# Kernel optimization log

Measured on AMD Instinct MI355X. Metric: run time of the kernel, lower is better.

## Reference

```python
import jax, jax.numpy as jnp
import numpy as np

S = 3
K = 3
K2 = K * K
BN_EPS = 1e-5


def _conv(x, w, pad=0):
    return jax.lax.conv_general_dilated(
        x, w, window_strides=(1, 1), padding=[(pad, pad), (pad, pad)],
        dimension_numbers=('NCHW', 'OIHW', 'NCHW'))


def _adaptive_avg_pool(x, s):
    # PyTorch adaptive_avg_pool2d semantics: bin i covers [floor(i*H/s), ceil((i+1)*H/s))
    B, C, H, W = x.shape
    rows = []
    for i in range(s):
        h0, h1 = (i * H) // s, -(-((i + 1) * H) // s)
        cols = []
        for j in range(s):
            w0, w1 = (j * W) // s, -(-((j + 1) * W) // s)
            cols.append(x[:, :, h0:h1, w0:w1].mean(axis=(2, 3)))
        rows.append(jnp.stack(cols, axis=-1))
    return jnp.stack(rows, axis=-2)  # (B, C, s, s)


def _forward(c4, c5, w_to_fuse, bn_gamma, bn_beta, w_c4_proc, w_conv1,
             w_reshape, w_proj, w_sim4, w_sim5, kg_w1, kg_b1, kg_w2, kg_b2,
             mask_raw):
    B, C4, H, W = c4.shape
    H2, W2 = c5.shape[2], c5.shape[3]
    # nearest upsample c5 -> (H, W)
    ih = (jnp.arange(H) * H2) // H
    iw = (jnp.arange(W) * W2) // W
    c5_up = c5[:, :, ih][:, :, :, iw]

    c4_proc = _conv(c4, w_c4_proc, pad=1)
    c5_proc = _conv(c5_up, w_conv1)  # adaptive pool to (H,W) is identity here
    fused = c4_proc + c5_proc

    # to_fuse 1x1 conv -> BatchNorm (training-mode batch stats) -> SiLU
    y = _conv(fused, w_to_fuse)
    mu = y.mean(axis=(0, 2, 3), keepdims=True)
    var = y.var(axis=(0, 2, 3), keepdims=True)
    y = (y - mu) / jnp.sqrt(var + BN_EPS)
    X = jax.nn.silu(y * bn_gamma[None, :, None, None] + bn_beta[None, :, None, None])

    # patch descriptors and similarity (dot)
    p4 = _conv(_adaptive_avg_pool(c4, S), w_sim4)    # (B, sim, S, S)
    p5 = _conv(_adaptive_avg_pool(c5_up, S), w_sim5)
    sim = (p4 * p5).sum(axis=1)                      # (B, S, S)

    gated = sim.reshape(B, S * S) * jax.nn.sigmoid(mask_raw)[None, :]  # (B, S2)
    k_in = gated.reshape(B * S * S, 1)
    h = jax.nn.relu(k_in @ kg_w1.T + kg_b1)
    kernels = jax.nn.softmax((h @ kg_w2.T + kg_b2).reshape(B, S * S, K2), axis=-1)

    # unfold X: (B, C, K2, H, W) with torch row-major kernel-position order
    pad = K // 2
    Xp = jnp.pad(X, ((0, 0), (0, 0), (pad, pad), (pad, pad)))
    patches = jnp.stack([Xp[:, :, dy:dy + H, dx:dx + W]
                         for dy in range(K) for dx in range(K)], axis=2)

    # per-pixel patch index -> per-pixel kernel
    y_idx = jnp.clip((jnp.arange(H) * S) // H, 0, S - 1)
    x_idx = jnp.clip((jnp.arange(W) * S) // W, 0, S - 1)
    pidx = y_idx[:, None] * S + x_idx[None, :]       # (H, W) int
    kmap = kernels[:, pidx, :]                       # (B, H, W, K2)

    out = jnp.einsum('bckhw,bhwk->bchw', patches, kmap)

    fused_red = _conv(_conv(fused, w_reshape), w_proj)
    return out + fused_red


def setup_inputs() -> dict:
    key = jax.random.key(0)
    ks = jax.random.split(key, 16)
    B, C4, C5, H, W = 8, 256, 512, 64, 64
    OC, SIM, FR, HID = 256, 64, 128, 16
    n = jax.random.normal
    return {
        'c4': n(ks[0], (B, C4, H, W), dtype=jnp.float32),
        'c5': n(ks[1], (B, C5, H // 2, W // 2), dtype=jnp.float32),
        'w_to_fuse': n(ks[2], (OC, C4, 1, 1), dtype=jnp.float32) * 0.05,
        'bn_gamma': jnp.ones((OC,), dtype=jnp.float32),
        'bn_beta': jnp.zeros((OC,), dtype=jnp.float32),
        'w_c4_proc': n(ks[3], (C4, C4, 3, 3), dtype=jnp.float32) * 0.05,
        'w_conv1': n(ks[4], (C4, C5, 1, 1), dtype=jnp.float32) * 0.05,
        'w_reshape': n(ks[5], (FR, C4, 1, 1), dtype=jnp.float32) * 0.05,
        'w_proj': n(ks[6], (OC, FR, 1, 1), dtype=jnp.float32) * 0.05,
        'w_sim4': n(ks[7], (SIM, C4, 1, 1), dtype=jnp.float32) * 0.05,
        'w_sim5': n(ks[8], (SIM, C5, 1, 1), dtype=jnp.float32) * 0.05,
        'kg_w1': n(ks[9], (HID, 1), dtype=jnp.float32) * 0.5,
        'kg_b1': n(ks[10], (HID,), dtype=jnp.float32) * 0.1,
        'kg_w2': n(ks[11], (K2, HID), dtype=jnp.float32) * 0.5,
        'kg_b2': n(ks[12], (K2,), dtype=jnp.float32) * 0.1,
        'mask_raw': jnp.zeros((K2,), dtype=jnp.float32),
    }


def reference(c4, c5, w_to_fuse, bn_gamma, bn_beta, w_c4_proc, w_conv1,
              w_reshape, w_proj, w_sim4, w_sim5, kg_w1, kg_b1, kg_w2, kg_b2,
              mask_raw):
    return _forward(c4, c5, w_to_fuse, bn_gamma, bn_beta, w_c4_proc, w_conv1,
                    w_reshape, w_proj, w_sim4, w_sim5, kg_w1, kg_b1, kg_w2,
                    kg_b2, mask_raw)
```

## Files before the change

kernel.cpp:

```cpp
#include <hip/hip_runtime.h>
#include <cstddef>

#define B_   8
#define C4_  256
#define C5_  512
#define OC_  256
#define FR_  128
#define H_   64
#define W_   64
#define HW_  4096

typedef unsigned short u16;
typedef __bf16 bf16x8 __attribute__((ext_vector_type(8)));
typedef float floatx16 __attribute__((ext_vector_type(16)));

__device__ __forceinline__ u16 f2b(float x) {
    unsigned int u = __float_as_uint(x);
    return (u16)((u + 0x7FFFu + ((u >> 16) & 1u)) >> 16);
}
__device__ __forceinline__ float b2f(u16 x) {
    return __uint_as_float(((unsigned int)x) << 16);
}

__device__ __forceinline__ void gll16(const u16* g, char* l) {
    __builtin_amdgcn_global_load_lds(
        (const __attribute__((address_space(1))) void*)g,
        (__attribute__((address_space(3))) void*)l, 16, 0, 0);
}

__global__ __launch_bounds__(256) void pack_all(
    const float* __restrict__ w3, const float* __restrict__ w1,
    const float* __restrict__ wtf,
    const float* __restrict__ wp, const float* __restrict__ wr,
    const float* __restrict__ in4, const float* __restrict__ in5,
    u16* __restrict__ A3f, u16* __restrict__ A1f, u16* __restrict__ Wtff,
    u16* __restrict__ Wefff, u16* __restrict__ c4t, u16* __restrict__ c5f,
    float* __restrict__ pool4, float* __restrict__ pool5)
{
    __shared__ float sT[16448];
    const int t = threadIdx.x;
    const int blk = blockIdx.x;

    if (blk < 3072) {
        int i = blk * 256 + t;
        if (i < 589824) {
            int j  = i & 7;
            int l  = (i >> 3) & 63;
            int ks = (i >> 9) & 15;
            int ot = (i >> 13) & 7;
            int tap = i >> 16;
            int oc = ot * 32 + (l & 31);
            int c  = ks * 16 + ((l >> 5) << 3) + j;
            A3f[i] = f2b(w3[((size_t)oc * 256 + c) * 9 + tap]);
        } else if (i < 720896) {
            int i2 = i - 589824;
            int j  = i2 & 7;
            int l  = (i2 >> 3) & 63;
            int ks = (i2 >> 9) & 31;
            int ot = i2 >> 14;
            int oc = ot * 32 + (l & 31);
            int c  = ks * 16 + ((l >> 5) << 3) + j;
            A1f[i2] = f2b(w1[(size_t)oc * 512 + c]);
        } else {
            int i3 = i - 720896;
            int j  = i3 & 7;
            int l  = (i3 >> 3) & 63;
            int ks = (i3 >> 9) & 15;
            int ot = i3 >> 13;
            int oc = ot * 32 + (l & 31);
            int c  = ks * 16 + ((l >> 5) << 3) + j;
            Wtff[i3] = f2b(wtf[(size_t)oc * 256 + c]);
        }
    } else if (blk < 3328) {
        const int oc = blk - 3072, c = t;
        float s = 0.f;
        for (int f = 0; f < 128; ++f)
            s += wp[oc * 128 + f] * wr[f * 256 + c];
        int ot = oc >> 5;
        int lf = (oc & 31) + (((c >> 3) & 1) << 5);
        int ks = c >> 4;
        int j  = c & 7;
        Wefff[(((size_t)ot * 16 + ks) * 64 + lf) * 8 + j] = f2b(s);
    } else {
        const int id = blk - 3328;
        const int b = id / 96, x = id % 96;
        if (x < 64) {
            const int h = x;
            const int w = t & 63, cg = t >> 6;
            for (int i = 0; i < 64; ++i) {
                int c = cg * 64 + i;
                sT[w * 257 + c] = in4[(((size_t)b * 256 + c) * 64 + h) * 64 + w];
            }
            __syncthreads();
            for (int i = 0; i < 16; ++i) {
                int ww = cg * 16 + i;
                int c0 = (t & 63) * 4;
                ushort4 v;
                v.x = f2b(sT[ww * 257 + c0]);
                v.y = f2b(sT[ww * 257 + c0 + 1]);
                v.z = f2b(sT[ww * 257 + c0 + 2]);
                v.w = f2b(sT[ww * 257 + c0 + 3]);
                *(ushort4*)&c4t[(((size_t)b * 66 + h + 1) * 72 + ww + 1) * 256 + c0] = v;
            }
            {
                const int c = t;
                float cs[3];
                #pragma unroll
                for (int j = 0; j < 3; ++j) {
                    const int w0 = (j * 64) / 3, w1 = ((j + 1) * 64 + 2) / 3;
                    float s = 0.f;
                    for (int w2 = w0; w2 < w1; ++w2) s += sT[w2 * 257 + c];
                    cs[j] = s;
                }
                #pragma unroll
                for (int i = 0; i < 3; ++i) {
                    const int h0 = (i * 64) / 3, h1 = ((i + 1) * 64 + 2) / 3;
                    if (h >= h0 && h < h1) {
                        #pragma unroll
                        for (int j = 0; j < 3; ++j)
                            atomicAdd(&pool4[((size_t)b * 256 + c) * 9 + i * 3 + j], cs[j]);
                    }
                }
            }
        } else {
            const int h2 = x - 64;
            const int w = t & 31, cg = t >> 5;
            for (int i = 0; i < 64; ++i) {
                int c = cg * 64 + i;
                sT[w * 513 + c] = in5[(((size_t)b * 512 + c) * 32 + h2) * 32 + w];
            }
            __syncthreads();
            u16* dstb = c5f + (size_t)(b * 32 + h2) * 32768;
            for (int i = 0; i < 32; ++i) {
                int id2 = i * 256 + t;
                int j0 = (id2 & 1) * 4;
                int l  = (id2 >> 1) & 63;
                int ks = (id2 >> 7) & 31;
                int n  = (id2 >> 12) & 1;
                int ch = ks * 16 + ((l >> 5) << 3) + j0;
                int w2 = (n * 32 + (l & 31)) >> 1;
                ushort4 v;
                v.x = f2b(sT[w2 * 513 + ch]);
                v.y = f2b(sT[w2 * 513 + ch + 1]);
                v.z = f2b(sT[w2 * 513 + ch + 2]);
                v.w = f2b(sT[w2 * 513 + ch + 3]);
                *(ushort4*)&dstb[id2 * 4] = v;
            }
            #pragma unroll
            for (int half = 0; half < 2; ++half) {
                const int cc = half * 256 + t;
                float cs[3];
                #pragma unroll
                for (int j = 0; j < 3; ++j) {
                    const int w0 = (j * 64) / 3, w1 = ((j + 1) * 64 + 2) / 3;
                    float s = 0.f;
                    for (int w2 = w0; w2 < w1; ++w2) s += sT[(w2 >> 1) * 513 + cc];
                    cs[j] = s;
                }
                #pragma unroll
                for (int i = 0; i < 3; ++i) {
                    const int h0 = (i * 64) / 3, h1 = ((i + 1) * 64 + 2) / 3;
                    const int wt = (int)(2 * h2 >= h0 && 2 * h2 < h1)
                                 + (int)(2 * h2 + 1 >= h0 && 2 * h2 + 1 < h1);
                    if (wt) {
                        const float fw = (float)wt;
                        #pragma unroll
                        for (int j = 0; j < 3; ++j)
                            atomicAdd(&pool5[((size_t)b * 512 + cc) * 9 + i * 3 + j], fw * cs[j]);
                    }
                }
            }
        }
    }
}

__global__ __launch_bounds__(512, 1) void fuse_all(
    const u16* __restrict__ c4t, const u16* __restrict__ c5f,
    const u16* __restrict__ A3f, const u16* __restrict__ A1f,
    const u16* __restrict__ Wtff, const u16* __restrict__ Wefff,
    u16* __restrict__ yb, u16* __restrict__ outb, float* __restrict__ sums)
{
    extern __shared__ char smem[];
    float* lsum = (float*)(smem + 73728);
    float* lsq  = lsum + 256;

    const int t   = threadIdx.x;
    const int lin = blockIdx.x;
    const int d   = ((lin & 7) << 5) + (lin >> 3);
    const int b   = d >> 5;
    const int rp  = d & 31;
    const int h0  = rp * 2;

    const int l   = t & 63;
    const int w8  = t >> 6;
    const int og  = w8 >> 1;
    const int pg  = w8 & 1;
    const int lc  = l & 31;
    const int lg  = l >> 5;

    const int ocb = og * 64;
    const int otb = og * 2;
    const int gseg = (l & 7) ^ (l >> 3);

    if (t < 256) { lsum[t] = 0.f; lsq[t] = 0.f; }

    floatx16 acc[2][2];
    #pragma unroll
    for (int m = 0; m < 2; ++m)
        #pragma unroll
        for (int n = 0; n < 2; ++n)
            #pragma unroll
            for (int r = 0; r < 16; ++r)
                acc[m][n][r] = 0.f;

    bf16x8 areg[9][2];
    #pragma unroll
    for (int tap = 0; tap < 9; ++tap)
        #pragma unroll
        for (int m = 0; m < 2; ++m)
            areg[tap][m] = *(const bf16x8*)(A3f + ((((size_t)tap * 8 + otb + m) * 16 + 0) * 64 + l) * 8);

    for (int q = w8; q < 36; q += 8) {
        const int r  = q / 9;
        const int cq = (q - r * 9) * 8;
        const u16* gp = c4t + ((((size_t)b * 66 + h0 + r) * 72 + cq + (l >> 3)) << 8)
                      + gseg * 8;
        gll16(gp, smem + (r * 72 + cq) * 128);
    }
    __syncthreads();

    for (int c0 = 0; c0 < 256; c0 += 64) {
        char* bufc = smem + ((c0 >> 6) & 1) * 36864;
        if (c0 < 192) {
            char* bufn = smem + (((c0 >> 6) + 1) & 1) * 36864;
            for (int q = w8; q < 36; q += 8) {
                const int r  = q / 9;
                const int cq = (q - r * 9) * 8;
                const u16* gp = c4t + ((((size_t)b * 66 + h0 + r) * 72 + cq + (l >> 3)) << 8)
                              + c0 + 64 + gseg * 8;
                gll16(gp, bufn + (r * 72 + cq) * 128);
            }
        }

        const int ksb = c0 >> 4;
        #pragma unroll
        for (int kst = 0; kst < 4; ++kst) {
            const int ksgN = (kst < 3) ? (ksb + kst + 1)
                                       : ((c0 < 192) ? ksb + 4 : 0);
            #pragma unroll
            for (int ky = 0; ky < 3; ++ky) {
                #pragma unroll
                for (int kx = 0; kx < 3; ++kx) {
                    const int tap = ky * 3 + kx;
                    bf16x8 bb[2];
                    #pragma unroll
                    for (int n = 0; n < 2; ++n) {
                        const int pix = (pg + ky) * 72 + n * 32 + lc + kx;
                        const int seg = (kst * 2 + lg) ^ (pix & 7);
                        bb[n] = *(const bf16x8*)(bufc + pix * 128 + (seg << 4));
                    }
                    #pragma unroll
                    for (int m = 0; m < 2; ++m)
                        #pragma unroll
                        for (int n = 0; n < 2; ++n)
                            acc[m][n] = __builtin_amdgcn_mfma_f32_32x32x16_bf16(
                                areg[tap][m], bb[n], acc[m][n], 0, 0, 0);
                    #pragma unroll
                    for (int m = 0; m < 2; ++m)
                        areg[tap][m] = *(const bf16x8*)(A3f + ((((size_t)tap * 8 + otb + m) * 16 + ksgN) * 64 + l) * 8);
                }
            }
        }
        __syncthreads();
    }

    const u16* c5b = c5f + (size_t)(b * 32 + rp) * 32768;
    {
        bf16x8 a1[2][2], b1[2][2];
        #pragma unroll
        for (int m = 0; m < 2; ++m) {
            a1[0][m] = *(const bf16x8*)(A1f + ((((size_t)otb + m) * 32 + 0) * 64 + l) * 8);
            b1[0][m] = *(const bf16x8*)(c5b + (((size_t)m * 32 + 0) * 64 + l) * 8);
        }
        #pragma unroll
        for (int ks = 0; ks < 32; ++ks) {
            const int cur = ks & 1, nxt = cur ^ 1;
            if (ks < 31) {
                #pragma unroll
                for (int m = 0; m < 2; ++m) {
                    a1[nxt][m] = *(const bf16x8*)(A1f + ((((size_t)otb + m) * 32 + ks + 1) * 64 + l) * 8);
                    b1[nxt][m] = *(const bf16x8*)(c5b + (((size_t)m * 32 + ks + 1) * 64 + l) * 8);
                }
            }
            #pragma unroll
            for (int m = 0; m < 2; ++m)
                #pragma unroll
                for (int n = 0; n < 2; ++n)
                    acc[m][n] = __builtin_amdgcn_mfma_f32_32x32x16_bf16(
                        a1[cur][m], b1[cur][n], acc[m][n], 0, 0, 0);
        }
    }

    __syncthreads();
    #pragma unroll
    for (int n = 0; n < 2; ++n) {
        const int px = pg * 64 + n * 32 + lc;
        #pragma unroll
        for (int m = 0; m < 2; ++m) {
            #pragma unroll
            for (int rq = 0; rq < 4; ++rq) {
                const int oc = ocb + m * 32 + rq * 8 + lg * 4;
                const int slot = oc >> 3;
                ushort4 v;
                v.x = f2b(acc[m][n][rq * 4 + 0]);
                v.y = f2b(acc[m][n][rq * 4 + 1]);
                v.z = f2b(acc[m][n][rq * 4 + 2]);
                v.w = f2b(acc[m][n][rq * 4 + 3]);
                *(ushort4*)(smem + px * 512 + ((slot ^ (px & 31)) << 4) + (oc & 7) * 2) = v;
            }
        }
    }
    __syncthreads();

    const bool isY = (w8 < 4);
    const u16* Wf  = isY ? Wtff : Wefff;
    u16* dst       = isY ? yb : outb;
    const int ot2  = (w8 & 3) * 2;

    #pragma unroll
    for (int ph = 0; ph < 2; ++ph) {
        floatx16 a2[2][2];
        #pragma unroll
        for (int m = 0; m < 2; ++m)
            #pragma unroll
            for (int n = 0; n < 2; ++n)
                #pragma unroll
                for (int r = 0; r < 16; ++r)
                    a2[m][n][r] = 0.f;

        bf16x8 wreg[2][2];
        #pragma unroll
        for (int m = 0; m < 2; ++m)
            wreg[0][m] = *(const bf16x8*)(Wf + ((((size_t)ot2 + m) * 16 + 0) * 64 + l) * 8);

        #pragma unroll
        for (int ks = 0; ks < 16; ++ks) {
            const int cur = ks & 1, nxt = cur ^ 1;
            if (ks < 15) {
                #pragma unroll
                for (int m = 0; m < 2; ++m)
                    wreg[nxt][m] = *(const bf16x8*)(Wf + ((((size_t)ot2 + m) * 16 + ks + 1) * 64 + l) * 8);
            }
            bf16x8 bb[2];
            #pragma unroll
            for (int n = 0; n < 2; ++n) {
                const int px = ph * 64 + n * 32 + lc;
                const int slot = ks * 2 + lg;
                bb[n] = *(const bf16x8*)(smem + px * 512 + ((slot ^ (px & 31)) << 4));
            }
            #pragma unroll
            for (int m = 0; m < 2; ++m)
                #pragma unroll
                for (int n = 0; n < 2; ++n)
                    a2[m][n] = __builtin_amdgcn_mfma_f32_32x32x16_bf16(
                        wreg[cur][m], bb[n], a2[m][n], 0, 0, 0);
        }

        #pragma unroll
        for (int n = 0; n < 2; ++n) {
            const int px = ph * 64 + n * 32 + lc;
            const int row = px >> 6, wcol = px & 63;
            const size_t gp = (((size_t)b * 64 + h0 + row) * 64 + wcol) * 256;
            #pragma unroll
            for (int m = 0; m < 2; ++m) {
                #pragma unroll
                for (int rq = 0; rq < 4; ++rq) {
                    const int ocl = (w8 & 3) * 64 + m * 32 + rq * 8 + lg * 4;
                    ushort4 v;
                    v.x = f2b(a2[m][n][rq * 4 + 0]);
                    v.y = f2b(a2[m][n][rq * 4 + 1]);
                    v.z = f2b(a2[m][n][rq * 4 + 2]);
                    v.w = f2b(a2[m][n][rq * 4 + 3]);
                    *(ushort4*)&dst[gp + ocl] = v;
                }
            }
        }

        if (isY) {
            #pragma unroll
            for (int m = 0; m < 2; ++m) {
                #pragma unroll
                for (int r = 0; r < 16; ++r) {
                    float s = 0.f, q = 0.f;
                    #pragma unroll
                    for (int n = 0; n < 2; ++n) {
                        float v = a2[m][n][r];
                        s += v; q += v * v;
                    }
                    #pragma unroll
                    for (int off = 1; off < 32; off <<= 1) {
                        s += __shfl_xor(s, off);
                        q += __shfl_xor(q, off);
                    }
                    if (lc == 0) {
                        const int ocl = (w8 & 3) * 64 + m * 32 + (r & 3) + 8 * (r >> 2) + 4 * lg;
                        atomicAdd(&lsum[ocl], s);
                        atomicAdd(&lsq[ocl], q);
                    }
                }
            }
        }
    }

    __syncthreads();
    if (t < 256) {
        atomicAdd(&sums[t], lsum[t]);
        atomicAdd(&sums[256 + t], lsq[t]);
    }
}

__global__ __launch_bounds__(64) void sim_mlp(
    const float* __restrict__ pool4, const float* __restrict__ pool5,
    const float* __restrict__ w4, const float* __restrict__ w5,
    const float* __restrict__ kgw1, const float* __restrict__ kgb1,
    const float* __restrict__ kgw2, const float* __restrict__ kgb2,
    const float* __restrict__ mask, float* __restrict__ kers)
{
    const int r = blockIdx.x, b = blockIdx.y, m = threadIdx.x;
    float p4 = 0.f, p5 = 0.f;
    for (int c = 0; c < C4_; ++c)
        p4 += w4[(size_t)m * C4_ + c] * pool4[((size_t)b * C4_ + c) * 9 + r];
    for (int c = 0; c < C5_; ++c)
        p5 += w5[(size_t)m * C5_ + c] * pool5[((size_t)b * C5_ + c) * 9 + r];
    float v = p4 * p5;
    #pragma unroll
    for (int off = 32; off; off >>= 1) v += __shfl_down(v, off);
    if (m == 0) {
        const int ri = r / 3, rj = r % 3;
        const int h0 = (ri * 64) / 3, h1 = ((ri + 1) * 64 + 2) / 3;
        const int w0 = (rj * 64) / 3, w1 = ((rj + 1) * 64 + 2) / 3;
        const float inv = 1.f / (float)((h1 - h0) * (w1 - w0));
        v *= inv * inv;
        float g = v * (1.f / (1.f + __expf(-mask[r])));
        float hb[16];
        #pragma unroll
        for (int j = 0; j < 16; ++j) hb[j] = fmaxf(g * kgw1[j] + kgb1[j], 0.f);
        float lg[9], mx = -1e30f;
        #pragma unroll
        for (int k = 0; k < 9; ++k) {
            float s = kgb2[k];
            #pragma unroll
            for (int j = 0; j < 16; ++j) s += kgw2[k * 16 + j] * hb[j];
            lg[k] = s;
            mx = fmaxf(mx, s);
        }
        float den = 0.f;
        #pragma unroll
        for (int k = 0; k < 9; ++k) { lg[k] = __expf(lg[k] - mx); den += lg[k]; }
        float inv2 = 1.f / den;
        #pragma unroll
        for (int k = 0; k < 9; ++k)
            kers[((size_t)b * 9 + r) * 9 + k] = lg[k] * inv2;
    }
}

__global__ __launch_bounds__(256) void dynconv_bn(const u16* __restrict__ yb,
                                                  const u16* __restrict__ outb,
                                                  const float* __restrict__ sums,
                                                  const float* __restrict__ gamma,
                                                  const float* __restrict__ beta,
                                                  const float* __restrict__ kers,
                                                  float* __restrict__ out)
{
    __shared__ float sX[4][10][66];
    __shared__ float sK[81];
    __shared__ float sAB[8];
    const int t = threadIdx.x;
    const int lin = blockIdx.x;
    const int dd  = ((lin & 7) << 9) | (lin >> 3);
    const int b   = dd >> 9;
    const int r0  = ((dd >> 6) & 7) * 8;
    const int cg  = dd & 63;
    const int ch = t >> 6, w = t & 63;
    const int c = cg * 4 + ch;

    if (t < 4) {
        const int cc = cg * 4 + t;
        const float n = (float)(B_ * HW_);
        float mu  = sums[cc] / n;
        float var = sums[256 + cc] / n - mu * mu;
        float a = gamma[cc] * rsqrtf(var + 1e-5f);
        sAB[t]     = a;
        sAB[4 + t] = beta[cc] - mu * a;
    }
    if (t < 81) sK[t] = kers[(size_t)b * 81 + t];
    __syncthreads();

    for (int idx = t; idx < 660; idx += 256) {
        int rr = idx / 66, cl = idx % 66;
        int gh = r0 - 1 + rr, gw = cl - 1;
        float v0 = 0.f, v1 = 0.f, v2 = 0.f, v3 = 0.f;
        if (gh >= 0 && gh < H_ && gw >= 0 && gw < W_) {
            ushort4 u = *(const ushort4*)&yb[((((size_t)b * 64 + gh) * 64 + gw) << 8) + cg * 4];
            float z;
            z = fmaf(sAB[0], b2f(u.x), sAB[4]); v0 = z / (1.f + __expf(-z));
            z = fmaf(sAB[1], b2f(u.y), sAB[5]); v1 = z / (1.f + __expf(-z));
            z = fmaf(sAB[2], b2f(u.z), sAB[6]); v2 = z / (1.f + __expf(-z));
            z = fmaf(sAB[3], b2f(u.w), sAB[7]); v3 = z / (1.f + __expf(-z));
        }
        sX[0][rr][cl] = v0;
        sX[1][rr][cl] = v1;
        sX[2][rr][cl] = v2;
        sX[3][rr][cl] = v3;
    }
    __syncthreads();

    const int rx = (w * 3) >> 6;
    for (int hh = 0; hh < 8; ++hh) {
        int h = r0 + hh;
        int ry = (h * 3) >> 6;
        const float* kp = &sK[(ry * 3 + rx) * 9];
        float acc = 0.f;
        #pragma unroll
        for (int dy = 0; dy < 3; ++dy)
            #pragma unroll
            for (int dx = 0; dx < 3; ++dx)
                acc += kp[dy * 3 + dx] * sX[ch][hh + dy][w + dx];
        acc += b2f(outb[((((size_t)b * 64 + h) * 64 + w) << 8) + c]);
        out[(((size_t)b * 256 + c) * H_ + h) * W_ + w] = acc;
    }
}

extern "C" void kernel_launch(void* const* d_in, const int* in_sizes, int n_in,
                              void* d_out, int out_size, void* d_ws, size_t ws_size,
                              hipStream_t stream)
{
    const float* c4       = (const float*)d_in[0];
    const float* c5       = (const float*)d_in[1];
    const float* w_to_fuse= (const float*)d_in[2];
    const float* bn_gamma = (const float*)d_in[3];
    const float* bn_beta  = (const float*)d_in[4];
    const float* w_c4_proc= (const float*)d_in[5];
    const float* w_conv1  = (const float*)d_in[6];
    const float* w_reshape= (const float*)d_in[7];
    const float* w_proj   = (const float*)d_in[8];
    const float* w_sim4   = (const float*)d_in[9];
    const float* w_sim5   = (const float*)d_in[10];
    const float* kg_w1    = (const float*)d_in[11];
    const float* kg_b1    = (const float*)d_in[12];
    const float* kg_w2    = (const float*)d_in[13];
    const float* kg_b2    = (const float*)d_in[14];
    const float* mask_raw = (const float*)d_in[15];

    float* out = (float*)d_out;

    u16*   yb    = (u16*)d_ws;
    u16*   outb  = yb + 8388608;
    u16*   c4t   = outb + 8388608;
    u16*   c5f   = c4t + 9732096;
    u16*   A3f   = c5f + 8388608;
    u16*   A1f   = A3f + 589824;
    u16*   Wtff  = A1f + 131072;
    u16*   Wefff = Wtff + 65536;
    float* pool4 = (float*)(Wefff + 65536);
    float* pool5 = pool4 + 18432;
    float* sums  = pool5 + 36864;
    float* kers  = sums + 512;

    hipMemsetAsync(pool4, 0, (size_t)(18432 + 36864 + 512) * sizeof(float), stream);
    hipMemsetAsync(c4t, 0, (size_t)9732096 * sizeof(u16), stream);

    pack_all<<<4096, 256, 0, stream>>>(w_c4_proc, w_conv1, w_to_fuse,
                                       w_proj, w_reshape, c4, c5,
                                       A3f, A1f, Wtff, Wefff, c4t, c5f,
                                       pool4, pool5);

    fuse_all<<<256, 512, 75776, stream>>>(c4t, c5f, A3f, A1f, Wtff, Wefff,
                                          yb, outb, sums);

    sim_mlp<<<dim3(9, 8), 64, 0, stream>>>(pool4, pool5, w_sim4, w_sim5,
                                           kg_w1, kg_b1, kg_w2, kg_b2,
                                           mask_raw, kers);

    dynconv_bn<<<4096, 256, 0, stream>>>(yb, outb, sums,
                                         bn_gamma, bn_beta, kers, out);
}
```

Measured before the change: 219.9 us.

## Split fused conv kernel to one output row per block, doubling grid

Each fuse_all block now handles a single image row (64 pixels) instead of two, so the grid goes from 256 to 512 blocks. The per-warp tile shrinks from 2x2 to 2x1 MFMA tiles in the 3x3 and c5 stages, the halo buffer shrinks to 3 rows, and the epilogue phase loop collapses to one pass. Launch bounds allow more blocks per CU to raise occupancy and spread work over all CUs. In exchange the 3x3 halo rows (3 per output row instead of 4 per two) and the weight fragments are reloaded more often relative to the compute, lowering reuse.

```diff
diff --git a/kernel.cpp b/kernel.cpp
--- a/kernel.cpp
+++ b/kernel.cpp
@@ -174,44 +174,40 @@
     }
 }
 
-__global__ __launch_bounds__(512, 1) void fuse_all(
+__global__ __launch_bounds__(512, 4) void fuse_all(
     const u16* __restrict__ c4t, const u16* __restrict__ c5f,
     const u16* __restrict__ A3f, const u16* __restrict__ A1f,
     const u16* __restrict__ Wtff, const u16* __restrict__ Wefff,
     u16* __restrict__ yb, u16* __restrict__ outb, float* __restrict__ sums)
 {
     extern __shared__ char smem[];
-    float* lsum = (float*)(smem + 73728);
+    float* lsum = (float*)(smem + 55296);
     float* lsq  = lsum + 256;
 
     const int t   = threadIdx.x;
     const int lin = blockIdx.x;
-    const int d   = ((lin & 7) << 5) + (lin >> 3);
-    const int b   = d >> 5;
-    const int rp  = d & 31;
-    const int h0  = rp * 2;
+    const int d   = ((lin & 7) << 6) + (lin >> 3);
+    const int b   = d >> 6;
+    const int h   = d & 63;
 
     const int l   = t & 63;
     const int w8  = t >> 6;
-    const int og  = w8 >> 1;
-    const int pg  = w8 & 1;
+    const int og  = w8 & 3;
+    const int pxh = w8 >> 2;
     const int lc  = l & 31;
     const int lg  = l >> 5;
 
-    const int ocb = og * 64;
     const int otb = og * 2;
     const int gseg = (l & 7) ^ (l >> 3);
 
     if (t < 256) { lsum[t] = 0.f; lsq[t] = 0.f; }
 
-    floatx16 acc[2][2];
+    floatx16 acc[2];
     #pragma unroll
     for (int m = 0; m < 2; ++m)
         #pragma unroll
-        for (int n = 0; n < 2; ++n)
-            #pragma unroll
-            for (int r = 0; r < 16; ++r)
-                acc[m][n][r] = 0.f;
+        for (int r = 0; r < 16; ++r)
+            acc[m][r] = 0.f;
 
     bf16x8 areg[9][2];
     #pragma unroll
@@ -220,23 +216,23 @@
         for (int m = 0; m < 2; ++m)
             areg[tap][m] = *(const bf16x8*)(A3f + ((((size_t)tap * 8 + otb + m) * 16 + 0) * 64 + l) * 8);
 
-    for (int q = w8; q < 36; q += 8) {
+    for (int q = w8; q < 27; q += 8) {
         const int r  = q / 9;
         const int cq = (q - r * 9) * 8;
-        const u16* gp = c4t + ((((size_t)b * 66 + h0 + r) * 72 + cq + (l >> 3)) << 8)
+        const u16* gp = c4t + ((((size_t)b * 66 + h + r) * 72 + cq + (l >> 3)) << 8)
                       + gseg * 8;
         gll16(gp, smem + (r * 72 + cq) * 128);
     }
     __syncthreads();
 
     for (int c0 = 0; c0 < 256; c0 += 64) {
-        char* bufc = smem + ((c0 >> 6) & 1) * 36864;
+        char* bufc = smem + ((c0 >> 6) & 1) * 27648;
         if (c0 < 192) {
-            char* bufn = smem + (((c0 >> 6) + 1) & 1) * 36864;
-            for (int q = w8; q < 36; q += 8) {
+            char* bufn = smem + (((c0 >> 6) + 1) & 1) * 27648;
+            for (int q = w8; q < 27; q += 8) {
                 const int r  = q / 9;
                 const int cq = (q - r * 9) * 8;
-                const u16* gp = c4t + ((((size_t)b * 66 + h0 + r) * 72 + cq + (l >> 3)) << 8)
+                const u16* gp = c4t + ((((size_t)b * 66 + h + r) * 72 + cq + (l >> 3)) << 8)
                               + c0 + 64 + gseg * 8;
                 gll16(gp, bufn + (r * 72 + cq) * 128);
             }
@@ -252,19 +248,13 @@
                 #pragma unroll
                 for (int kx = 0; kx < 3; ++kx) {
                     const int tap = ky * 3 + kx;
-                    bf16x8 bb[2];
-                    #pragma unroll
-                    for (int n = 0; n < 2; ++n) {
-                        const int pix = (pg + ky) * 72 + n * 32 + lc + kx;
-                        const int seg = (kst * 2 + lg) ^ (pix & 7);
-                        bb[n] = *(const bf16x8*)(bufc + pix * 128 + (seg << 4));
-                    }
+                    const int pix = ky * 72 + pxh * 32 + lc + kx;
+                    const int seg = (kst * 2 + lg) ^ (pix & 7);
+                    bf16x8 bb = *(const bf16x8*)(bufc + pix * 128 + (seg << 4));
                     #pragma unroll
                     for (int m = 0; m < 2; ++m)
-                        #pragma unroll
-                        for (int n = 0; n < 2; ++n)
-                            acc[m][n] = __builtin_amdgcn_mfma_f32_32x32x16_bf16(
-                                areg[tap][m], bb[n], acc[m][n], 0, 0, 0);
+                        acc[m] = __builtin_amdgcn_mfma_f32_32x32x16_bf16(
+                            areg[tap][m], bb, acc[m], 0, 0, 0);
                     #pragma unroll
                     for (int m = 0; m < 2; ++m)
                         areg[tap][m] = *(const bf16x8*)(A3f + ((((size_t)tap * 8 + otb + m) * 16 + ksgN) * 64 + l) * 8);
@@ -274,48 +264,43 @@
         __syncthreads();
     }
 
-    const u16* c5b = c5f + (size_t)(b * 32 + rp) * 32768;
+    const u16* c5b = c5f + (size_t)(b * 32 + (h >> 1)) * 32768;
     {
-        bf16x8 a1[2][2], b1[2][2];
-        #pragma unroll
-        for (int m = 0; m < 2; ++m) {
+        bf16x8 a1[2][2], b1[2];
+        #pragma unroll
+        for (int m = 0; m < 2; ++m)
             a1[0][m] = *(const bf16x8*)(A1f + ((((size_t)otb + m) * 32 + 0) * 64 + l) * 8);
-            b1[0][m] = *(const bf16x8*)(c5b + (((size_t)m * 32 + 0) * 64 + l) * 8);
-        }
+        b1[0] = *(const bf16x8*)(c5b + (((size_t)pxh * 32 + 0) * 64 + l) * 8);
         #pragma unroll
         for (int ks = 0; ks < 32; ++ks) {
             const int cur = ks & 1, nxt = cur ^ 1;
             if (ks < 31) {
                 #pragma unroll
-                for (int m = 0; m < 2; ++m) {
+                for (int m = 0; m < 2; ++m)
                     a1[nxt][m] = *(const bf16x8*)(A1f + ((((size_t)otb + m) * 32 + ks + 1) * 64 + l) * 8);
-                    b1[nxt][m] = *(const bf16x8*)(c5b + (((size_t)m * 32 + ks + 1) * 64 + l) * 8);
-                }
+                b1[nxt] = *(const bf16x8*)(c5b + (((size_t)pxh * 32 + ks + 1) * 64 + l) * 8);
             }
             #pragma unroll
             for (int m = 0; m < 2; ++m)
-                #pragma unroll
-                for (int n = 0; n < 2; ++n)
-                    acc[m][n] = __builtin_amdgcn_mfma_f32_32x32x16_bf16(
-                        a1[cur][m], b1[cur][n], acc[m][n], 0, 0, 0);
+                acc[m] = __builtin_amdgcn_mfma_f32_32x32x16_bf16(
+                    a1[cur][m], b1[cur], acc[m], 0, 0, 0);
         }
     }
 
     __syncthreads();
-    #pragma unroll
-    for (int n = 0; n < 2; ++n) {
-        const int px = pg * 64 + n * 32 + lc;
+    {
+        const int px = pxh * 32 + lc;
         #pragma unroll
         for (int m = 0; m < 2; ++m) {
             #pragma unroll
             for (int rq = 0; rq < 4; ++rq) {
-                const int oc = ocb + m * 32 + rq * 8 + lg * 4;
+                const int oc = og * 64 + m * 32 + rq * 8 + lg * 4;
                 const int slot = oc >> 3;
                 ushort4 v;
-                v.x = f2b(acc[m][n][rq * 4 + 0]);
-                v.y = f2b(acc[m][n][rq * 4 + 1]);
-                v.z = f2b(acc[m][n][rq * 4 + 2]);
-                v.w = f2b(acc[m][n][rq * 4 + 3]);
+                v.x = f2b(acc[m][rq * 4 + 0]);
+                v.y = f2b(acc[m][rq * 4 + 1]);
+                v.z = f2b(acc[m][rq * 4 + 2]);
+                v.w = f2b(acc[m][rq * 4 + 3]);
                 *(ushort4*)(smem + px * 512 + ((slot ^ (px & 31)) << 4) + (oc & 7) * 2) = v;
             }
         }
@@ -327,17 +312,16 @@
     u16* dst       = isY ? yb : outb;
     const int ot2  = (w8 & 3) * 2;
 
+    floatx16 a2[2][2];
     #pragma unroll
-    for (int ph = 0; ph < 2; ++ph) {
-        floatx16 a2[2][2];
-        #pragma unroll
-        for (int m = 0; m < 2; ++m)
-            #pragma unroll
-            for (int n = 0; n < 2; ++n)
-                #pragma unroll
-                for (int r = 0; r < 16; ++r)
-                    a2[m][n][r] = 0.f;
-
+    for (int m = 0; m < 2; ++m)
+        #pragma unroll
+        for (int n = 0; n < 2; ++n)
+            #pragma unroll
+            for (int r = 0; r < 16; ++r)
+                a2[m][n][r] = 0.f;
+
+    {
         bf16x8 wreg[2][2];
         #pragma unroll
         for (int m = 0; m < 2; ++m)
@@ -354,7 +338,7 @@
             bf16x8 bb[2];
             #pragma unroll
             for (int n = 0; n < 2; ++n) {
-                const int px = ph * 64 + n * 32 + lc;
+                const int px = n * 32 + lc;
                 const int slot = ks * 2 + lg;
                 bb[n] = *(const bf16x8*)(smem + px * 512 + ((slot ^ (px & 31)) << 4));
             }
@@ -365,48 +349,47 @@
                     a2[m][n] = __builtin_amdgcn_mfma_f32_32x32x16_bf16(
                         wreg[cur][m], bb[n], a2[m][n], 0, 0, 0);
         }
-
-        #pragma unroll
-        for (int n = 0; n < 2; ++n) {
-            const int px = ph * 64 + n * 32 + lc;
-            const int row = px >> 6, wcol = px & 63;
-            const size_t gp = (((size_t)b * 64 + h0 + row) * 64 + wcol) * 256;
-            #pragma unroll
-            for (int m = 0; m < 2; ++m) {
-                #pragma unroll
-                for (int rq = 0; rq < 4; ++rq) {
-                    const int ocl = (w8 & 3) * 64 + m * 32 + rq * 8 + lg * 4;
-                    ushort4 v;
-                    v.x = f2b(a2[m][n][rq * 4 + 0]);
-                    v.y = f2b(a2[m][n][rq * 4 + 1]);
-                    v.z = f2b(a2[m][n][rq * 4 + 2]);
-                    v.w = f2b(a2[m][n][rq * 4 + 3]);
-                    *(ushort4*)&dst[gp + ocl] = v;
-                }
-            }
-        }
-
-        if (isY) {
-            #pragma unroll
-            for (int m = 0; m < 2; ++m) {
-                #pragma unroll
-                for (int r = 0; r < 16; ++r) {
-                    float s = 0.f, q = 0.f;
-                    #pragma unroll
-                    for (int n = 0; n < 2; ++n) {
-                        float v = a2[m][n][r];
-                        s += v; q += v * v;
-                    }
-                    #pragma unroll
-                    for (int off = 1; off < 32; off <<= 1) {
-                        s += __shfl_xor(s, off);
-                        q += __shfl_xor(q, off);
-                    }
-                    if (lc == 0) {
-                        const int ocl = (w8 & 3) * 64 + m * 32 + (r & 3) + 8 * (r >> 2) + 4 * lg;
-                        atomicAdd(&lsum[ocl], s);
-                        atomicAdd(&lsq[ocl], q);
-                    }
+    }
+
+    #pragma unroll
+    for (int n = 0; n < 2; ++n) {
+        const int wcol = n * 32 + lc;
+        const size_t gp = (((size_t)b * 64 + h) * 64 + wcol) * 256;
+        #pragma unroll
+        for (int m = 0; m < 2; ++m) {
+            #pragma unroll
+            for (int rq = 0; rq < 4; ++rq) {
+                const int ocl = (w8 & 3) * 64 + m * 32 + rq * 8 + lg * 4;
+                ushort4 v;
+                v.x = f2b(a2[m][n][rq * 4 + 0]);
+                v.y = f2b(a2[m][n][rq * 4 + 1]);
+                v.z = f2b(a2[m][n][rq * 4 + 2]);
+                v.w = f2b(a2[m][n][rq * 4 + 3]);
+                *(ushort4*)&dst[gp + ocl] = v;
+            }
+        }
+    }
+
+    if (isY) {
+        #pragma unroll
+        for (int m = 0; m < 2; ++m) {
+            #pragma unroll
+            for (int r = 0; r < 16; ++r) {
+                float s = 0.f, q = 0.f;
+                #pragma unroll
+                for (int n = 0; n < 2; ++n) {
+                    float v = a2[m][n][r];
+                    s += v; q += v * v;
+                }
+                #pragma unroll
+                for (int off = 1; off < 32; off <<= 1) {
+                    s += __shfl_xor(s, off);
+                    q += __shfl_xor(q, off);
+                }
+                if (lc == 0) {
+                    const int ocl = (w8 & 3) * 64 + m * 32 + (r & 3) + 8 * (r >> 2) + 4 * lg;
+                    atomicAdd(&lsum[ocl], s);
+                    atomicAdd(&lsq[ocl], q);
                 }
             }
         }
@@ -575,7 +558,7 @@
                                        A3f, A1f, Wtff, Wefff, c4t, c5f,
                                        pool4, pool5);
 
-    fuse_all<<<256, 512, 75776, stream>>>(c4t, c5f, A3f, A1f, Wtff, Wefff,
+    fuse_all<<<512, 512, 57344, stream>>>(c4t, c5f, A3f, A1f, Wtff, Wefff,
                                           yb, outb, sums);
 
     sim_mlp<<<dim3(9, 8), 64, 0, stream>>>(pool4, pool5, w_sim4, w_sim5,
```

Result: slower. 238.1 us (+8.3%).
